# Optimization experiments

Measured on AMD Instinct MI355X. Metric: run time of the kernel, lower is better.

## Reference

```python
import jax, jax.numpy as jnp
import numpy as np

D = 512      # d_model
H = 8        # n_head
L = 6        # n_layers
DFF = 2048   # d_inner
V = 10000    # vocab
NPOS = 2048
B, T = 8, 1023
S = 1024     # encoder length


def sinusoid_table(n_position, d_hid):
    pos = np.arange(n_position)[:, None].astype(np.float64)
    i = np.arange(d_hid)[None, :]
    angle = pos / np.power(10000.0, 2 * (i // 2) / d_hid)
    tab = np.zeros((n_position, d_hid))
    tab[:, 0::2] = np.sin(angle[:, 0::2])
    tab[:, 1::2] = np.cos(angle[:, 1::2])
    return jnp.asarray(tab, jnp.float32)


def layer_norm(x, g, b, eps=1e-6):
    m = x.mean(-1, keepdims=True)
    v = x.var(-1, keepdims=True)
    return (x - m) / jnp.sqrt(v + eps) * g + b


def mha(x, kv, wq, wk, wv, wo, g, b, mask):
    # x: [B,Lq,D], kv: [B,Lk,D], mask: [B,Lq|1,Lk] int or None
    Bq, Lq, _ = x.shape
    Lk = kv.shape[1]
    dk = D // H
    q = (x @ wq).reshape(Bq, Lq, H, dk).transpose(0, 2, 1, 3)   # bhqd
    k = (kv @ wk).reshape(Bq, Lk, H, dk).transpose(0, 2, 1, 3)  # bhkd
    v = (kv @ wv).reshape(Bq, Lk, H, dk).transpose(0, 2, 1, 3)
    scores = jnp.einsum('bhqd,bhkd->bhqk', q, k) / jnp.sqrt(jnp.asarray(dk, x.dtype))
    if mask is not None:
        scores = jnp.where(mask[:, None, :, :] == 0, jnp.asarray(-1e9, x.dtype), scores)
    a = jax.nn.softmax(scores, axis=-1)
    o = jnp.einsum('bhqk,bhkd->bhqd', a, v).transpose(0, 2, 1, 3).reshape(Bq, Lq, D)
    o = o @ wo + x  # residual
    return layer_norm(o, g, b)


def ffn(x, w1, b1, w2, b2, g, b):
    h = jax.nn.relu(x @ w1 + b1)
    return layer_norm(h @ w2 + b2 + x, g, b)


def setup_inputs() -> dict:
    key = jax.random.key(0)
    ks = iter(jax.random.split(key, 64))
    sc = 0.02
    inp = {}
    inp['trg_seq'] = jax.random.randint(next(ks), (B, T), 0, V, dtype=jnp.int32)
    # causal mask over decoder length T+1 (1 = attend)
    T1 = T + 1
    inp['trg_mask'] = jnp.tril(jnp.ones((T1, T1), jnp.int32))[None].repeat(B, axis=0)
    inp['enc_output'] = jax.random.normal(next(ks), (B, S, D), jnp.float32)
    inp['src_mask'] = jnp.ones((B, 1, S), jnp.int32)
    inp['emb'] = jax.random.normal(next(ks), (V, D), jnp.float32) * sc
    inp['ln0_g'] = jnp.ones((D,), jnp.float32)
    inp['ln0_b'] = jnp.zeros((D,), jnp.float32)
    for nm in ['wq_s', 'wk_s', 'wv_s', 'wo_s', 'wq_c', 'wk_c', 'wv_c', 'wo_c']:
        inp[nm] = jax.random.normal(next(ks), (L, D, D), jnp.float32) * sc
    for nm in ['ln1_g', 'ln2_g', 'ln3_g']:
        inp[nm] = jnp.ones((L, D), jnp.float32)
    for nm in ['ln1_b', 'ln2_b', 'ln3_b']:
        inp[nm] = jnp.zeros((L, D), jnp.float32)
    inp['w1'] = jax.random.normal(next(ks), (L, D, DFF), jnp.float32) * sc
    inp['b1'] = jnp.zeros((L, DFF), jnp.float32)
    inp['w2'] = jax.random.normal(next(ks), (L, DFF, D), jnp.float32) * sc
    inp['b2'] = jnp.zeros((L, D), jnp.float32)
    return inp


def reference(trg_seq, trg_mask, enc_output, src_mask, emb, ln0_g, ln0_b,
              wq_s, wk_s, wv_s, wo_s, ln1_g, ln1_b,
              wq_c, wk_c, wv_c, wo_c, ln2_g, ln2_b,
              w1, b1, w2, b2, ln3_g, ln3_b):
    Bq, Tq = trg_seq.shape
    tok = emb[trg_seq]                                         # [B,T,D]
    x = jnp.concatenate([jnp.zeros((Bq, 1, D), tok.dtype), tok], axis=1)  # [B,T+1,D]
    x = x + sinusoid_table(NPOS, D)[None, :Tq + 1]
    x = layer_norm(x, ln0_g, ln0_b)
    for l in range(L):
        x = mha(x, x, wq_s[l], wk_s[l], wv_s[l], wo_s[l], ln1_g[l], ln1_b[l], trg_mask)
        x = mha(x, enc_output, wq_c[l], wk_c[l], wv_c[l], wo_c[l], ln2_g[l], ln2_b[l], src_mask)
        x = ffn(x, w1[l], b1[l], w2[l], b2[l], ln3_g[l], ln3_b[l])
    return x
```

## Files before the change

kernel.cpp:

```cpp
#include <hip/hip_runtime.h>
#include <stdint.h>


typedef unsigned short u16;
typedef float floatx4 __attribute__((ext_vector_type(4)));
typedef short short8 __attribute__((ext_vector_type(8)));

__device__ __forceinline__ float b2f(u16 u) {
    union { unsigned int i; float f; } c; c.i = ((unsigned int)u) << 16; return c.f;
}
__device__ __forceinline__ u16 f2b(float f) {
    union { float f; unsigned int i; } c; c.f = f;
    return (u16)((c.i + 0x7FFFu + ((c.i >> 16) & 1u)) >> 16);
}
__device__ __forceinline__ float ldf(const void* p, size_t i, bool is32) {
    return is32 ? ((const float*)p)[i] : b2f(((const u16*)p)[i]);
}
__device__ __forceinline__ void async16(u16* lds, const u16* g) {
    __builtin_amdgcn_global_load_lds(
        (const __attribute__((address_space(1))) unsigned int*)g,
        (__attribute__((address_space(3))) unsigned int*)lds, 16, 0, 0);
}
__device__ __forceinline__ void xcd_remap(int gx, int gy, int& bx, int& by) {
    const int fid = bx + gx * by;
    const int xcd = fid & 7;
    const int i = fid >> 3;
    bx = i % gx;
    by = xcd * (gy >> 3) + i / gx;
}

__global__ __launch_bounds__(256)
void conv_bf16_kernel(const void* __restrict__ src, u16* __restrict__ dst,
                      const u16* __restrict__ probe)
{
    const bool is32 = (probe[0] == 0);
    const size_t off = ((size_t)blockIdx.x * 256 + threadIdx.x) * 4;
    u16 o[4];
    if (is32) {
        float4 f = *(const float4*)((const float*)src + off);
        o[0] = f2b(f.x); o[1] = f2b(f.y); o[2] = f2b(f.z); o[3] = f2b(f.w);
    } else {
        uint2 vv = *(const uint2*)((const u16*)src + off);
        const u16* pv = (const u16*)&vv;
        o[0] = pv[0]; o[1] = pv[1]; o[2] = pv[2]; o[3] = pv[3];
    }
    *(uint2*)&dst[off] = *(uint2*)o;
}

__global__ __launch_bounds__(256)
void transpose_layer_kernel(const void* __restrict__ wq_s, const void* __restrict__ wk_s,
                            const void* __restrict__ wv_s, const void* __restrict__ wo_s,
                            const void* __restrict__ wq_c, const void* __restrict__ wk_c,
                            const void* __restrict__ wv_c, const void* __restrict__ wo_c,
                            const void* __restrict__ w1,   const void* __restrict__ w2,
                            u16* __restrict__ wT, const u16* __restrict__ probe,
                            size_t loff2, size_t loff1)
{
    __shared__ u16 tile[32][33];
    const bool is32 = (probe[0] == 0);
    const int bid = blockIdx.x;
    const int tid = threadIdx.x;
    const void* src; u16* dst; int C, R, tr, tc; size_t loff;
    if (bid < 2048) {
        const int mat = bid >> 8, t = bid & 255;
        R = 512; C = 512; tr = t >> 4; tc = t & 15; loff = loff2;
        const void* tbl[8] = {wq_s, wk_s, wv_s, wo_s, wq_c, wk_c, wv_c, wo_c};
        src = tbl[mat]; dst = wT + (size_t)mat * 262144;
    } else if (bid < 3072) {
        const int t = bid - 2048;
        R = 512; C = 2048; tr = t >> 6; tc = t & 63; loff = loff1;
        src = w1; dst = wT + 2097152;
    } else {
        const int t = bid - 3072;
        R = 2048; C = 512; tr = t >> 4; tc = t & 15; loff = loff1;
        src = w2; dst = wT + 3145728;
    }
    const int r = tid >> 3, c0 = (tid & 7) * 4;
    const size_t off = loff + (size_t)(tr * 32 + r) * C + tc * 32 + c0;
    u16 vals[4];
    if (is32) {
        float4 f = *(const float4*)((const float*)src + off);
        vals[0] = f2b(f.x); vals[1] = f2b(f.y); vals[2] = f2b(f.z); vals[3] = f2b(f.w);
    } else {
        uint2 vv = *(const uint2*)((const u16*)src + off);
        const u16* pv = (const u16*)&vv;
        vals[0] = pv[0]; vals[1] = pv[1]; vals[2] = pv[2]; vals[3] = pv[3];
    }
#pragma unroll
    for (int j = 0; j < 4; j++) tile[r][c0 + j] = vals[j];
    __syncthreads();
    uint2 ov; u16* po = (u16*)&ov;
#pragma unroll
    for (int j = 0; j < 4; j++) po[j] = tile[c0 + j][r];
    *(uint2*)&dst[(size_t)(tc * 32 + r) * R + tr * 32 + c0] = ov;
}

template<int EPI>
__global__ __launch_bounds__(512)
void gemm256(const u16* __restrict__ A, const u16* __restrict__ Bt,
             const void* __restrict__ bias, size_t boff,
             u16* __restrict__ outb, u16* __restrict__ out1, u16* __restrict__ out2,
             const u16* __restrict__ probe, int M, int N, int K)
{
    __shared__ u16 As[2][256 * 64];
    __shared__ u16 Bs[2][256 * 64];
    const int tid = threadIdx.x;
    const int lane = tid & 63;
    const int quad = lane >> 4, cl = lane & 15;
    const int wave = tid >> 6;
    const int wm2 = (wave >> 2) * 128;
    const int wn2 = (wave & 3) * 64;
    int bx = blockIdx.x, by = blockIdx.y;
    xcd_remap(gridDim.x, gridDim.y, bx, by);
    const int m0 = by * 256, n0 = bx * 256;

    floatx4 acc[8][4];
#pragma unroll
    for (int i = 0; i < 8; i++)
#pragma unroll
        for (int j = 0; j < 4; j++)
#pragma unroll
            for (int r = 0; r < 4; r++) acc[i][j][r] = 0.0f;

    const int lrow = lane >> 3;
    const int lcol = ((lane & 7) ^ lrow) * 8;
    const u16* gA = &A [(size_t)(m0 + wave * 8 + lrow) * K + lcol];
    const u16* gB = &Bt[(size_t)(n0 + wave * 8 + lrow) * K + lcol];

    auto stage = [&](int bsel, int k0) {
#pragma unroll
        for (int s = 0; s < 4; s++)
            async16(&As[bsel][(s * 64 + wave * 8) * 64], gA + (size_t)s * 64 * K + k0);
#pragma unroll
        for (int s = 0; s < 4; s++)
            async16(&Bs[bsel][(s * 64 + wave * 8) * 64], gB + (size_t)s * 64 * K + k0);
    };

    const int nkt = K >> 6;
    stage(0, 0);
    stage(1, 64);

    const int c7 = cl & 7;
    for (int t = 0; t < nkt; ++t) {
        const int cur = t & 1;
        if (t == nkt - 1) asm volatile("s_waitcnt vmcnt(0)" ::: "memory");
        else              asm volatile("s_waitcnt vmcnt(8)" ::: "memory");
        __builtin_amdgcn_sched_barrier(0);
        __builtin_amdgcn_s_barrier();

        const u16* Ac = As[cur];
        const u16* Bc = Bs[cur];
#pragma unroll
        for (int kk = 0; kk < 2; kk++) {
            const int gsw = ((kk * 4 + quad) ^ c7) * 8;
            short8 af[8], bf[4];
#pragma unroll
            for (int mi = 0; mi < 8; mi++)
                af[mi] = *(const short8*)&Ac[(wm2 + mi * 16 + cl) * 64 + gsw];
#pragma unroll
            for (int ni = 0; ni < 4; ni++)
                bf[ni] = *(const short8*)&Bc[(wn2 + ni * 16 + cl) * 64 + gsw];
#pragma unroll
            for (int mi = 0; mi < 8; mi++)
#pragma unroll
                for (int ni = 0; ni < 4; ni++)
                    acc[mi][ni] = __builtin_amdgcn_mfma_f32_16x16x32_bf16(af[mi], bf[ni], acc[mi][ni], 0, 0, 0);
        }
        __builtin_amdgcn_s_barrier();
        __builtin_amdgcn_sched_barrier(0);
        if (t + 2 < nkt) stage(cur, (t + 2) * 64);
    }

    const bool is32 = (probe[0] == 0);
#pragma unroll
    for (int mi = 0; mi < 8; mi++) {
#pragma unroll
        for (int ni = 0; ni < 4; ni++) {
            const int col = n0 + wn2 + ni * 16 + cl;
            const float bv = ldf(bias, boff + col, is32);
#pragma unroll
            for (int r = 0; r < 4; r++) {
                const int row = m0 + wm2 + mi * 16 + quad * 4 + r;
                float v = acc[mi][ni][r] + bv;
                v = fmaxf(v, 0.0f);
                outb[(size_t)row * N + col] = f2b(v);
            }
        }
    }
}

template<int EPI>
__global__ __launch_bounds__(256)
void gemm_bf16(const u16* __restrict__ A, const u16* __restrict__ Bt,
               const void* __restrict__ bias, size_t boff, float* __restrict__ resid,
               u16* __restrict__ outb, u16* __restrict__ out1, u16* __restrict__ out2,
               const u16* __restrict__ probe, int M, int N, int K)
{
    __shared__ u16 As[3][128 * 32];
    __shared__ u16 Bs[3][128 * 32];
    const int tid = threadIdx.x;
    const int lane = tid & 63;
    const int quad = lane >> 4, cl = lane & 15;
    const int wave = tid >> 6;
    const int wm = (wave >> 1) * 64, wn = (wave & 1) * 64;
    int bx = blockIdx.x, by = blockIdx.y;
    xcd_remap(gridDim.x, gridDim.y, bx, by);
    const int m0 = by * 128, n0 = bx * 128;

    const u16* Ause = A;
    if (EPI == 4) {
        const u16* A2 = (const u16*)bias;
        if (A2 != nullptr && n0 >= 512) Ause = A2;
    }

    floatx4 acc[4][4];
#pragma unroll
    for (int i = 0; i < 4; i++)
#pragma unroll
        for (int j = 0; j < 4; j++)
#pragma unroll
            for (int r = 0; r < 4; r++) acc[i][j][r] = 0.0f;

    const int srow = tid >> 2;
    const int scol = (((tid & 3) ^ ((srow >> 1) & 3))) * 8;
    const int rslot = (quad ^ ((cl >> 1) & 3)) * 8;
    const int Ksub = K / gridDim.z;
    const int kbeg = blockIdx.z * Ksub, kend = kbeg + Ksub;
    const int nsteps = (kend - kbeg) >> 5;

    const u16* ga0 = &Ause[(size_t)(m0 + srow) * K + scol];
    const u16* ga1 = &Ause[(size_t)(m0 + 64 + srow) * K + scol];
    const u16* gb0 = &Bt[(size_t)(n0 + srow) * K + scol];
    const u16* gb1 = &Bt[(size_t)(n0 + 64 + srow) * K + scol];

    auto stage = [&](int bsel, int kk) {
        async16(&As[bsel][wave * 512],        ga0 + kk);
        async16(&As[bsel][2048 + wave * 512], ga1 + kk);
        async16(&Bs[bsel][wave * 512],        gb0 + kk);
        async16(&Bs[bsel][2048 + wave * 512], gb1 + kk);
    };

    stage(0, kbeg);
    if (nsteps > 1) stage(1, kbeg + 32);

    for (int t = 0; t < nsteps; ++t) {
        const int cur = t % 3;
        if (t + 2 < nsteps) stage((t + 2) % 3, kbeg + (t + 2) * 32);
        const int rem = nsteps - 1 - t;
        if (rem >= 2)      asm volatile("s_waitcnt vmcnt(8)" ::: "memory");
        else if (rem == 1) asm volatile("s_waitcnt vmcnt(4)" ::: "memory");
        else               asm volatile("s_waitcnt vmcnt(0)" ::: "memory");
        __builtin_amdgcn_sched_barrier(0);
        __builtin_amdgcn_s_barrier();

        const u16* Ac = As[cur];
        const u16* Bc = Bs[cur];
        short8 af[4], bfr[4];
#pragma unroll
        for (int mi = 0; mi < 4; mi++) af[mi]  = *(const short8*)&Ac[(wm + mi * 16 + cl) * 32 + rslot];
#pragma unroll
        for (int ni = 0; ni < 4; ni++) bfr[ni] = *(const short8*)&Bc[(wn + ni * 16 + cl) * 32 + rslot];
#pragma unroll
        for (int mi = 0; mi < 4; mi++)
#pragma unroll
            for (int ni = 0; ni < 4; ni++)
                acc[mi][ni] = __builtin_amdgcn_mfma_f32_16x16x32_bf16(af[mi], bfr[ni], acc[mi][ni], 0, 0, 0);
        __builtin_amdgcn_s_barrier();
    }

    if (EPI == 4) {
        const int seg = n0 >> 9;
        const int cbase = (n0 & 511) + wn;
        if (seg < 2) {
            u16* dst = (seg == 0) ? outb : out1;
#pragma unroll
            for (int mi = 0; mi < 4; mi++)
#pragma unroll
                for (int ni = 0; ni < 4; ni++) {
                    const int c = cbase + ni * 16 + cl;
#pragma unroll
                    for (int r = 0; r < 4; r++)
                        dst[(size_t)(m0 + wm + mi * 16 + quad * 4 + r) * 512 + c] = f2b(acc[mi][ni][r]);
                }
        } else {
            u16* dst = out2;
#pragma unroll
            for (int mi = 0; mi < 4; mi++) {
                const int row0 = m0 + wm + mi * 16 + quad * 4;
                const int b8 = (row0 >> 10) * 8;
                const int key0 = row0 & 1023;
#pragma unroll
                for (int ni = 0; ni < 4; ni++) {
                    const int c = cbase + ni * 16 + cl;
                    u16 pk[4];
#pragma unroll
                    for (int r = 0; r < 4; r++) pk[r] = f2b(acc[mi][ni][r]);
                    const size_t vrow = (size_t)(b8 + (c >> 6)) * 64 + (c & 63);
                    *(uint2*)&dst[vrow * 1024 + key0] = *(uint2*)pk;
                }
            }
        }
        return;
    }

    bool is32 = false;
    if (EPI == 1 || EPI == 2 || EPI == 3) is32 = (probe[0] == 0);
    const bool addbias = (bias != nullptr) && (blockIdx.z == 0);
    float* pslice = (EPI == 3) ? resid + (size_t)blockIdx.z * M * N : resid;
#pragma unroll
    for (int mi = 0; mi < 4; mi++) {
#pragma unroll
        for (int ni = 0; ni < 4; ni++) {
            const int col = n0 + wn + ni * 16 + cl;
#pragma unroll
            for (int r = 0; r < 4; r++) {
                const int row = m0 + wm + mi * 16 + quad * 4 + r;
                float v = acc[mi][ni][r];
                if (EPI == 1) { v += ldf(bias, boff + col, is32); v = fmaxf(v, 0.0f); }
                if (EPI == 2) {
                    if (addbias) v += ldf(bias, boff + col, is32);
                    atomicAdd(&resid[(size_t)row * N + col], v);
                } else if (EPI == 3) {
                    if (addbias) v += ldf(bias, boff + col, is32);
                    pslice[(size_t)row * N + col] = v;
                } else {
                    outb[(size_t)row * N + col] = f2b(v);
                }
            }
        }
    }
}

template<int CAUSAL>
__global__ __launch_bounds__(512)
void attn_kernel(const u16* __restrict__ Q, const u16* __restrict__ Kb,
                 const u16* __restrict__ VT, u16* __restrict__ O)
{
    __shared__ u16 Kt[2][64][72];
    __shared__ u16 Vt[2][64][72];
    int bx = blockIdx.x, bh = blockIdx.y;
    xcd_remap(gridDim.x, gridDim.y, bx, bh);
    const int b = bh >> 3, h = bh & 7;
    const int tid = threadIdx.x;
    const int w = tid >> 6;
    const int lane = tid & 63;
    const int quad = lane >> 4, cl = lane & 15;

    const int sA = bx;
    const int sB = CAUSAL ? (7 - bx) : (bx + 4);
    const int limA = CAUSAL ? (2 * bx + 2) : 16;
    const int nkt  = CAUSAL ? (16 - 2 * bx) : 16;

    const size_t qhd = (size_t)(b * 1024) * 512 + h * 64;
    const size_t qrA = qhd + (size_t)(sA * 128 + w * 16 + cl) * 512;
    const size_t qrB = qhd + (size_t)(sB * 128 + w * 16 + cl) * 512;
    const short8 qfA0 = *(const short8*)&Q[qrA + quad * 8];
    const short8 qfA1 = *(const short8*)&Q[qrA + 32 + quad * 8];
    const short8 qfB0 = *(const short8*)&Q[qrB + quad * 8];
    const short8 qfB1 = *(const short8*)&Q[qrB + 32 + quad * 8];
    const int qgA = sA * 128 + w * 16 + cl;
    const int qgB = sB * 128 + w * 16 + cl;

    float lsA = 0.0f, lsB = 0.0f;
    floatx4 oaccA[4], oaccB[4];
#pragma unroll
    for (int nb = 0; nb < 4; nb++)
#pragma unroll
        for (int r = 0; r < 4; r++) { oaccA[nb][r] = 0.0f; oaccB[nb][r] = 0.0f; }

    const int trow = tid >> 3, tcol = (tid & 7) * 8;
    const int tv = tid & 7;
    const int vm = (tv >> 2) * 32 + (tv & 1) * 16 + ((tv >> 1) & 1) * 4;
    const size_t kbase = (size_t)(b * 1024) * 512 + h * 64;
    const size_t vbase = (size_t)(bh * 64) * 1024;

    auto strip = [&](int cur, int k0, const short8& q0, const short8& q1,
                     int qg, float& ls, floatx4 (&oa)[4], bool msk) {
        floatx4 sacc[4];
#pragma unroll
        for (int kb2 = 0; kb2 < 4; kb2++)
#pragma unroll
            for (int r = 0; r < 4; r++) sacc[kb2][r] = 0.0f;
#pragma unroll
        for (int kb2 = 0; kb2 < 4; kb2++) {
            const short8 kf0 = *(const short8*)&Kt[cur][kb2 * 16 + cl][quad * 8];
            const short8 kf1 = *(const short8*)&Kt[cur][kb2 * 16 + cl][32 + quad * 8];
            sacc[kb2] = __builtin_amdgcn_mfma_f32_16x16x32_bf16(kf0, q0, sacc[kb2], 0, 0, 0);
            sacc[kb2] = __builtin_amdgcn_mfma_f32_16x16x32_bf16(kf1, q1, sacc[kb2], 0, 0, 0);
        }
        float p[4][4];
#pragma unroll
        for (int kb2 = 0; kb2 < 4; kb2++) {
#pragma unroll
            for (int r = 0; r < 4; r++) {
                float e = __expf(sacc[kb2][r] * 0.125f);
                if (msk) {
                    const int key = k0 + kb2 * 16 + quad * 4 + r;
                    e = (key > qg) ? 0.0f : e;
                }
                p[kb2][r] = e;
                ls += e;
            }
        }
        unsigned int pk[4][2];
#pragma unroll
        for (int kb2 = 0; kb2 < 4; kb2++) {
            asm("v_cvt_pk_bf16_f32 %0, %1, %2" : "=v"(pk[kb2][0]) : "v"(p[kb2][0]), "v"(p[kb2][1]));
            asm("v_cvt_pk_bf16_f32 %0, %1, %2" : "=v"(pk[kb2][1]) : "v"(p[kb2][2]), "v"(p[kb2][3]));
        }
#pragma unroll
        for (int c = 0; c < 2; c++) {
            union { short8 s8; unsigned int u[4]; } pa;
            pa.u[0] = pk[2 * c][0];     pa.u[1] = pk[2 * c][1];
            pa.u[2] = pk[2 * c + 1][0]; pa.u[3] = pk[2 * c + 1][1];
#pragma unroll
            for (int nb = 0; nb < 4; nb++) {
                const short8 vf = *(const short8*)&Vt[cur][nb * 16 + cl][c * 32 + quad * 8];
                oa[nb] = __builtin_amdgcn_mfma_f32_16x16x32_bf16(pa.s8, vf, oa[nb], 0, 0, 0);
            }
        }
    };

    uint4 ka = *(const uint4*)&Kb[kbase + (size_t)trow * 512 + tcol];
    uint4 va = *(const uint4*)&VT[vbase + (size_t)trow * 1024 + tcol];

    for (int kt = 0; kt < nkt; kt++) {
        const int cur = kt & 1;
        asm volatile("s_waitcnt vmcnt(0)" ::: "memory");
        *(uint4*)&Kt[cur][trow][tcol]   = ka;
        *(uint2*)&Vt[cur][trow][vm]     = make_uint2(va.x, va.y);
        *(uint2*)&Vt[cur][trow][vm + 8] = make_uint2(va.z, va.w);
        if (kt + 1 < nkt) {
            const int k1 = (kt + 1) * 64;
            ka = *(const uint4*)&Kb[kbase + (size_t)(k1 + trow) * 512 + tcol];
            va = *(const uint4*)&VT[vbase + (size_t)trow * 1024 + k1 + tcol];
        }
        asm volatile("s_waitcnt lgkmcnt(0)" ::: "memory");
        __builtin_amdgcn_sched_barrier(0);
        __builtin_amdgcn_s_barrier();
        __builtin_amdgcn_sched_barrier(0);

        const int k0 = kt * 64;
        strip(cur, k0, qfB0, qfB1, qgB, lsB, oaccB, CAUSAL && (kt >= nkt - 2));
        if (kt < limA)
            strip(cur, k0, qfA0, qfA1, qgA, lsA, oaccA, CAUSAL && (kt >= limA - 2));
    }
    lsA += __shfl_xor(lsA, 16, 64); lsA += __shfl_xor(lsA, 32, 64);
    lsB += __shfl_xor(lsB, 16, 64); lsB += __shfl_xor(lsB, 32, 64);
    float invA[4], invB[4];
#pragma unroll
    for (int r = 0; r < 4; r++) {
        invA[r] = 1.0f / __shfl(lsA, quad * 4 + r, 64);
        invB[r] = 1.0f / __shfl(lsB, quad * 4 + r, 64);
    }
    const size_t orA = (size_t)(b * 1024 + sA * 128 + w * 16 + quad * 4);
    const size_t orB = (size_t)(b * 1024 + sB * 128 + w * 16 + quad * 4);
#pragma unroll
    for (int nb = 0; nb < 4; nb++) {
#pragma unroll
        for (int r = 0; r < 4; r++) {
            O[(orA + r) * 512 + h * 64 + nb * 16 + cl] = f2b(oaccA[nb][r] * invA[r]);
            O[(orB + r) * 512 + h * 64 + nb * 16 + cl] = f2b(oaccB[nb][r] * invB[r]);
        }
    }
}

__device__ __forceinline__ float2 block_ln_512(float v0, float v1,
                                               float g0, float g1, float b0, float b1,
                                               int tid)
{
    __shared__ float red[8];
    float s = v0 + v1, sq = v0 * v0 + v1 * v1;
#pragma unroll
    for (int m = 1; m < 64; m <<= 1) { s += __shfl_xor(s, m, 64); sq += __shfl_xor(sq, m, 64); }
    const int wv = tid >> 6;
    if ((tid & 63) == 0) { red[wv * 2] = s; red[wv * 2 + 1] = sq; }
    __syncthreads();
    s  = red[0] + red[2] + red[4] + red[6];
    sq = red[1] + red[3] + red[5] + red[7];
    const float mean = s * (1.0f / 512.0f);
    const float var = sq * (1.0f / 512.0f) - mean * mean;
    const float rstd = rsqrtf(var + 1e-6f);
    return make_float2((v0 - mean) * rstd * g0 + b0, (v1 - mean) * rstd * g1 + b1);
}

__global__ __launch_bounds__(256)
void ln_kernel(float* __restrict__ xf, const void* __restrict__ g, const void* __restrict__ bb,
               size_t goff, const u16* __restrict__ probe,
               u16* __restrict__ xb, void* __restrict__ finalout,
               const float* __restrict__ p0, const float* __restrict__ p1)
{
    const bool is32 = (probe[0] == 0);
    const int row = blockIdx.x, tid = threadIdx.x;
    const int i = tid * 2;
    const size_t base = (size_t)row * 512;
    float2 v = *(const float2*)&xf[base + i];
    if (p0) {
        const float2 a = *(const float2*)&p0[base + i];
        v.x += a.x; v.y += a.y;
    }
    if (p1) {
        const float2 b = *(const float2*)&p1[base + i];
        v.x += b.x; v.y += b.y;
    }
    const float2 y = block_ln_512(v.x, v.y, ldf(g, goff + i, is32), ldf(g, goff + i + 1, is32),
                                  ldf(bb, goff + i, is32), ldf(bb, goff + i + 1, is32), tid);
    if (finalout) {
        if (is32) {
            *(float2*)&((float*)finalout)[base + i] = y;
        } else {
            u16* ob = (u16*)finalout;
            ob[base + i] = f2b(y.x); ob[base + i + 1] = f2b(y.y);
        }
    } else {
        *(float2*)&xf[base + i] = y;
        xb[base + i] = f2b(y.x); xb[base + i + 1] = f2b(y.y);
    }
}

__global__ __launch_bounds__(256)
void embed_ln_kernel(const int* __restrict__ trg_seq, const void* __restrict__ emb,
                     const void* __restrict__ g, const void* __restrict__ bb,
                     const u16* __restrict__ probe,
                     float* __restrict__ xf, u16* __restrict__ xb)
{
    const bool is32 = (probe[0] == 0);
    const int row = blockIdx.x;
    const int b = row >> 10, t = row & 1023;
    const int tid = threadIdx.x;
    const int tok = (t == 0) ? -1 : trg_seq[b * 1023 + t - 1];
    const int i = tid * 2;
    const float freq = __expf((float)i * (-9.210340371976184f / 512.0f));
    const float angle = (float)t * freq;
    float v0 = sinf(angle), v1 = cosf(angle);
    if (tok >= 0) {
        v0 += ldf(emb, (size_t)tok * 512 + i, is32);
        v1 += ldf(emb, (size_t)tok * 512 + i + 1, is32);
    }
    const float2 y = block_ln_512(v0, v1, ldf(g, i, is32), ldf(g, i + 1, is32),
                                  ldf(bb, i, is32), ldf(bb, i + 1, is32), tid);
    const size_t base = (size_t)row * 512;
    *(float2*)&xf[base + i] = y;
    xb[base + i] = f2b(y.x); xb[base + i + 1] = f2b(y.y);
}

extern "C" void kernel_launch(void* const* d_in, const int* in_sizes, int n_in,
                              void* d_out, int out_size, void* d_ws, size_t ws_size,
                              hipStream_t stream)
{
    const int* trg_seq = (const int*)d_in[0];
    const void* enc   = d_in[2];
    const void* emb   = d_in[4];
    const void* ln0_g = d_in[5];
    const void* ln0_b = d_in[6];
    const u16* probe  = (const u16*)d_in[5];

    char* ws = (char*)d_ws;
    float* xf   = (float*)(ws);
    u16*   xb   = (u16*)  (ws + (16u << 20));
    u16*   qb   = (u16*)  (ws + (24u << 20));
    u16*   kb   = (u16*)  (ws + (32u << 20));
    u16*   vt   = (u16*)  (ws + (40u << 20));
    u16*   ao   = (u16*)  (ws + (48u << 20));
    u16*   hb   = (u16*)  (ws + (24u << 20));
    u16*   wT   = (u16*)  (ws + (56u << 20));
    u16*   encb = (u16*)  (ws + (64u << 20));
    const bool bigws = ws_size >= (108ull << 20);
    float* p0 = (float*)(ws + (72u << 20));
    float* p1 = (float*)(ws + (88u << 20));
    const float* lp0 = bigws ? p0 : nullptr;
    const float* lp1 = bigws ? p1 : nullptr;

    const size_t E2 = 262144, E1 = 1048576;
    const dim3 gqkv(12, 64);
    const dim3 gffn1(8, 32);
    const dim3 gproj(4, 64);
    const dim3 gffn2(4, 64, 2);
    const dim3 gattn(4, 64);

    conv_bf16_kernel<<<4096, 256, 0, stream>>>(enc, encb, probe);
    embed_ln_kernel<<<8192, 256, 0, stream>>>(trg_seq, emb, ln0_g, ln0_b, probe, xf, xb);

    for (int l = 0; l < 6; l++) {
        transpose_layer_kernel<<<4096, 256, 0, stream>>>(
            d_in[7], d_in[8], d_in[9], d_in[10], d_in[11], d_in[12], d_in[13], d_in[14],
            d_in[21], d_in[23], wT, probe, (size_t)l * E2, (size_t)l * E1);

        gemm_bf16<4><<<gqkv, 256, 0, stream>>>(xb, wT, xb, 0, nullptr,
                                               qb, kb, vt, probe, 8192, 1536, 512);
        attn_kernel<1><<<gattn, 512, 0, stream>>>(qb, kb, vt, ao);
        if (bigws)
            gemm_bf16<3><<<gproj, 256, 0, stream>>>(ao, wT + 3 * E2, nullptr, 0, p0,
                                                    nullptr, nullptr, nullptr, probe, 8192, 512, 512);
        else
            gemm_bf16<2><<<gproj, 256, 0, stream>>>(ao, wT + 3 * E2, nullptr, 0, xf,
                                                    nullptr, nullptr, nullptr, probe, 8192, 512, 512);
        ln_kernel<<<8192, 256, 0, stream>>>(xf, d_in[15], d_in[18], (size_t)l * 512, probe, xb,
                                            nullptr, lp0, nullptr);

        gemm_bf16<4><<<gqkv, 256, 0, stream>>>(xb, wT + 4 * E2, encb, 0, nullptr,
                                               qb, kb, vt, probe, 8192, 1536, 512);
        attn_kernel<0><<<gattn, 512, 0, stream>>>(qb, kb, vt, ao);
        if (bigws)
            gemm_bf16<3><<<gproj, 256, 0, stream>>>(ao, wT + 7 * E2, nullptr, 0, p0,
                                                    nullptr, nullptr, nullptr, probe, 8192, 512, 512);
        else
            gemm_bf16<2><<<gproj, 256, 0, stream>>>(ao, wT + 7 * E2, nullptr, 0, xf,
                                                    nullptr, nullptr, nullptr, probe, 8192, 512, 512);
        ln_kernel<<<8192, 256, 0, stream>>>(xf, d_in[16], d_in[19], (size_t)l * 512, probe, xb,
                                            nullptr, lp0, nullptr);

        gemm256<1><<<gffn1, 512, 0, stream>>>(xb, wT + 2097152, d_in[22], (size_t)l * 2048,
                                              hb, nullptr, nullptr, probe, 8192, 2048, 512);
        if (bigws)
            gemm_bf16<3><<<gffn2, 256, 0, stream>>>(hb, wT + 3145728, d_in[24], (size_t)l * 512, p0,
                                                    nullptr, nullptr, nullptr, probe, 8192, 512, 2048);
        else
            gemm_bf16<2><<<gffn2, 256, 0, stream>>>(hb, wT + 3145728, d_in[24], (size_t)l * 512, xf,
                                                    nullptr, nullptr, nullptr, probe, 8192, 512, 2048);
        ln_kernel<<<8192, 256, 0, stream>>>(xf, d_in[17], d_in[20], (size_t)l * 512, probe, xb,
                                            (l == 5) ? d_out : nullptr, lp0, lp1);
    }
}
```

Baseline: 1.561 ms.

## Split GEMM k-loop into four phased MFMA clusters with priority and occupancy hint

Restructures the inner k-tile loop of the 256x256 GEMM into four phases. Each phase loads half the A fragments and reuses B fragments in registers, then issues a cluster of MFMAs under raised wave priority, with barriers between phases. The next tile's async global-to-LDS stage is issued before the last MFMA cluster so the load overlaps compute. A launch_bounds hint of 2 blocks per SM is added, which caps registers and may cause spills, and the extra barriers add sync overhead.

```diff
diff --git a/kernel.cpp b/kernel.cpp
--- a/kernel.cpp
+++ b/kernel.cpp
@@ -96,7 +96,7 @@
 }
 
 template<int EPI>
-__global__ __launch_bounds__(512)
+__global__ __launch_bounds__(512, 2)
 void gemm256(const u16* __restrict__ A, const u16* __restrict__ Bt,
              const void* __restrict__ bias, size_t boff,
              u16* __restrict__ outb, u16* __restrict__ out1, u16* __restrict__ out2,
@@ -141,34 +141,75 @@
     stage(1, 64);
 
     const int c7 = cl & 7;
+    const int g0 = (quad ^ c7) * 8;
+    const int g1 = ((4 + quad) ^ c7) * 8;
+
     for (int t = 0; t < nkt; ++t) {
         const int cur = t & 1;
+        const u16* Ac = As[cur];
+        const u16* Bc = Bs[cur];
+        short8 bf[4], af[4], ah[4];
+
         if (t == nkt - 1) asm volatile("s_waitcnt vmcnt(0)" ::: "memory");
         else              asm volatile("s_waitcnt vmcnt(8)" ::: "memory");
         __builtin_amdgcn_sched_barrier(0);
         __builtin_amdgcn_s_barrier();
-
-        const u16* Ac = As[cur];
-        const u16* Bc = Bs[cur];
-#pragma unroll
-        for (int kk = 0; kk < 2; kk++) {
-            const int gsw = ((kk * 4 + quad) ^ c7) * 8;
-            short8 af[8], bf[4];
-#pragma unroll
-            for (int mi = 0; mi < 8; mi++)
-                af[mi] = *(const short8*)&Ac[(wm2 + mi * 16 + cl) * 64 + gsw];
+#pragma unroll
+        for (int ni = 0; ni < 4; ni++) bf[ni] = *(const short8*)&Bc[(wn2 + ni * 16 + cl) * 64 + g0];
+#pragma unroll
+        for (int mi = 0; mi < 4; mi++) af[mi] = *(const short8*)&Ac[(wm2 + mi * 16 + cl) * 64 + g0];
+        asm volatile("s_waitcnt lgkmcnt(0)" ::: "memory");
+        __builtin_amdgcn_sched_barrier(0);
+        __builtin_amdgcn_s_setprio(1);
+#pragma unroll
+        for (int mi = 0; mi < 4; mi++)
 #pragma unroll
             for (int ni = 0; ni < 4; ni++)
-                bf[ni] = *(const short8*)&Bc[(wn2 + ni * 16 + cl) * 64 + gsw];
-#pragma unroll
-            for (int mi = 0; mi < 8; mi++)
-#pragma unroll
-                for (int ni = 0; ni < 4; ni++)
-                    acc[mi][ni] = __builtin_amdgcn_mfma_f32_16x16x32_bf16(af[mi], bf[ni], acc[mi][ni], 0, 0, 0);
-        }
-        __builtin_amdgcn_s_barrier();
-        __builtin_amdgcn_sched_barrier(0);
+                acc[mi][ni] = __builtin_amdgcn_mfma_f32_16x16x32_bf16(af[mi], bf[ni], acc[mi][ni], 0, 0, 0);
+        __builtin_amdgcn_s_setprio(0);
+        __builtin_amdgcn_s_barrier();
+
+#pragma unroll
+        for (int mi = 0; mi < 4; mi++) ah[mi] = *(const short8*)&Ac[(wm2 + (mi + 4) * 16 + cl) * 64 + g0];
+        asm volatile("s_waitcnt lgkmcnt(0)" ::: "memory");
+        __builtin_amdgcn_sched_barrier(0);
+        __builtin_amdgcn_s_setprio(1);
+#pragma unroll
+        for (int mi = 0; mi < 4; mi++)
+#pragma unroll
+            for (int ni = 0; ni < 4; ni++)
+                acc[mi + 4][ni] = __builtin_amdgcn_mfma_f32_16x16x32_bf16(ah[mi], bf[ni], acc[mi + 4][ni], 0, 0, 0);
+        __builtin_amdgcn_s_setprio(0);
+        __builtin_amdgcn_s_barrier();
+
+#pragma unroll
+        for (int ni = 0; ni < 4; ni++) bf[ni] = *(const short8*)&Bc[(wn2 + ni * 16 + cl) * 64 + g1];
+#pragma unroll
+        for (int mi = 0; mi < 4; mi++) af[mi] = *(const short8*)&Ac[(wm2 + mi * 16 + cl) * 64 + g1];
+        asm volatile("s_waitcnt lgkmcnt(0)" ::: "memory");
+        __builtin_amdgcn_sched_barrier(0);
+        __builtin_amdgcn_s_setprio(1);
+#pragma unroll
+        for (int mi = 0; mi < 4; mi++)
+#pragma unroll
+            for (int ni = 0; ni < 4; ni++)
+                acc[mi][ni] = __builtin_amdgcn_mfma_f32_16x16x32_bf16(af[mi], bf[ni], acc[mi][ni], 0, 0, 0);
+        __builtin_amdgcn_s_setprio(0);
+        __builtin_amdgcn_s_barrier();
+
+#pragma unroll
+        for (int mi = 0; mi < 4; mi++) ah[mi] = *(const short8*)&Ac[(wm2 + (mi + 4) * 16 + cl) * 64 + g1];
+        asm volatile("s_waitcnt lgkmcnt(0)" ::: "memory");
+        __builtin_amdgcn_sched_barrier(0);
+        __builtin_amdgcn_s_barrier();
         if (t + 2 < nkt) stage(cur, (t + 2) * 64);
+        __builtin_amdgcn_s_setprio(1);
+#pragma unroll
+        for (int mi = 0; mi < 4; mi++)
+#pragma unroll
+            for (int ni = 0; ni < 4; ni++)
+                acc[mi + 4][ni] = __builtin_amdgcn_mfma_f32_16x16x32_bf16(ah[mi], bf[ni], acc[mi + 4][ni], 0, 0, 0);
+        __builtin_amdgcn_s_setprio(0);
     }
 
     const bool is32 = (probe[0] == 0);
```

Result: no change. 1.566 ms (+0.3%).
